# Optimization experiments

Measured on AMD Instinct MI355X. Metric: run time of the kernel, lower is better.

Reference implementation:

```python
import jax, jax.numpy as jnp
import numpy as np

MASK_WEIGHT = 1.0
HEAD_DIM = 64
SCALING = HEAD_DIM ** -0.5


def _rotate_half(x):
    x1, x2 = jnp.split(x, 2, axis=-1)
    return jnp.concatenate([-x2, x1], axis=-1)


def _rope_tables(seq_len, dim, dtype):
    inv_freq = 1.0 / (10000.0 ** (jnp.arange(0, dim, 2, dtype=jnp.float32) / dim))
    t = jnp.arange(seq_len, dtype=jnp.float32)
    freqs = jnp.outer(t, inv_freq)                      # (s, d/2)
    cos = jnp.tile(jnp.cos(freqs), (1, 2)).astype(dtype)  # (s, d)  '(2 d)' tiling
    sin = jnp.tile(jnp.sin(freqs), (1, 2)).astype(dtype)
    return cos, sin


def _apply_rope(x, cos, sin):
    # x: (b, h, s, d); cos/sin: (s, d) broadcast over b, h
    return x * cos + _rotate_half(x) * sin


def setup_inputs() -> dict:
    key = jax.random.key(0)
    ks = jax.random.split(key, 6)
    b, h, s, d = 2, 16, 2048, 64
    d_model = h * d
    return {
        "q": jax.random.normal(ks[0], (b, h, s, d), jnp.float32),
        "k": jax.random.normal(ks[1], (b, h, s, d), jnp.float32),
        "v": jax.random.normal(ks[2], (b, h, s, d), jnp.float32),
        "attention_mask": jax.random.normal(ks[3], (1, h, s, s), jnp.float32) * 0.05,
        "out_w": jax.random.normal(ks[4], (d_model, d_model), jnp.float32) * (d_model ** -0.5),
        "out_b": jax.random.normal(ks[5], (d_model,), jnp.float32) * 0.02,
    }


def reference(q, k, v, attention_mask, out_w, out_b):
    b, h, s, d = q.shape
    cos, sin = _rope_tables(s, d, q.dtype)
    qr = _apply_rope(q, cos, sin)
    kr = _apply_rope(k, cos, sin)
    # learned per-head affinity transform of the queries: q' = (mask_weight * W) @ q
    W = attention_mask[0] * MASK_WEIGHT                    # (h, s, s), shared over batch
    qt = jnp.einsum('hqk,bhkd->bhqd', W, qr)
    # flash-style online softmax over keys == plain stable softmax (same math)
    scores = jnp.einsum('bhqd,bhkd->bhqk', qt, kr) * SCALING
    attn = jax.nn.softmax(scores, axis=-1)
    ctx = jnp.einsum('bhqk,bhkd->bhqd', attn, v)
    ctx = ctx.transpose(0, 2, 1, 3).reshape(b, s, h * d)   # (b, s, d_model)
    return ctx @ out_w.T + out_b
```

## Files before the change

### kernel.cpp

```cpp
#include <hip/hip_runtime.h>
#include <hip/hip_bf16.h>
#include <math.h>

typedef __bf16 bf16_t;
typedef __bf16 bf16x4 __attribute__((ext_vector_type(4)));
typedef __bf16 bf16x8 __attribute__((ext_vector_type(8)));
typedef float f32x4 __attribute__((ext_vector_type(4)));

#define NB 2
#define NH 16
#define SEQ 2048
#define HD 64
#define DMODEL 1024
#define QK_SCALE 0.125f
#define LOG2E 1.44269504088896340f
#define INV_2PI 0.15915494309189535f

__device__ __forceinline__ bf16_t to_bf16(float x) { return (bf16_t)x; }
#define MFMA16 __builtin_amdgcn_mfma_f32_16x16x32_bf16

__global__ __launch_bounds__(256) void k1_rope_pack(
    const float* __restrict__ q, const float* __restrict__ k, const float* __restrict__ v,
    bf16_t* __restrict__ qrT, bf16_t* __restrict__ krN, bf16_t* __restrict__ vT)
{
  __shared__ bf16_t tile[64][65];
  const int tid = threadIdx.x;
  const int blk = blockIdx.x;
  const int st = blk & 31;
  const int bh = blk >> 5;
  const int s0 = st * 64;

  const size_t base_sd = ((size_t)bh * SEQ + s0) * HD;
  const float* qb = q + base_sd;
  const float* kb = k + base_sd;
  const float* vb = v + base_sd;
  bf16_t* qrTb = qrT + (size_t)bh * HD * SEQ;
  bf16_t* krNb = krN + base_sd;
  bf16_t* vTb  = vT  + (size_t)bh * HD * SEQ;

  #pragma unroll
  for (int pp = 0; pp < 8; ++pp) {
    int idx = pp * 256 + tid;
    int sr = idx >> 5;
    int j  = idx & 31;
    float freq = __builtin_amdgcn_exp2f(-(float)j * (13.287712379549449f / 32.0f));
    float ang = (float)(s0 + sr) * freq;
    float rev = ang * INV_2PI;
    rev = rev - floorf(rev);
    float c  = __builtin_amdgcn_cosf(rev);
    float sn = __builtin_amdgcn_sinf(rev);
    float q1 = qb[sr*HD + j], q2 = qb[sr*HD + j + 32];
    tile[sr][j]      = to_bf16((q1*c - q2*sn) * QK_SCALE);
    tile[sr][j + 32] = to_bf16((q2*c + q1*sn) * QK_SCALE);
    float ka = kb[sr*HD + j], kbv = kb[sr*HD + j + 32];
    krNb[sr*HD + j]      = to_bf16(ka*c - kbv*sn);
    krNb[sr*HD + j + 32] = to_bf16(kbv*c + ka*sn);
  }
  __syncthreads();
  #pragma unroll
  for (int c = 0; c < 2; ++c) {
    int id = c*256 + tid;
    int d = id >> 3;
    int sc = (id & 7) * 8;
    bf16x8 vec;
    #pragma unroll
    for (int i = 0; i < 8; ++i) vec[i] = tile[sc + i][d];
    *(bf16x8*)&qrTb[(size_t)d * SEQ + s0 + sc] = vec;
  }
  __syncthreads();
  #pragma unroll
  for (int c = 0; c < 4; ++c) {
    int id = c*256 + tid;
    int sr = id >> 4;
    int c4 = (id & 15) * 4;
    float4 v4 = *(const float4*)&vb[sr*HD + c4];
    tile[sr][c4+0] = to_bf16(v4.x);
    tile[sr][c4+1] = to_bf16(v4.y);
    tile[sr][c4+2] = to_bf16(v4.z);
    tile[sr][c4+3] = to_bf16(v4.w);
  }
  __syncthreads();
  #pragma unroll
  for (int c = 0; c < 2; ++c) {
    int id = c*256 + tid;
    int d = id >> 3;
    int sc = (id & 7) * 8;
    bf16x8 vec;
    #pragma unroll
    for (int i = 0; i < 8; ++i) vec[i] = tile[sc + i][d];
    *(bf16x8*)&vTb[(size_t)d * SEQ + s0 + sc] = vec;
  }
}

__global__ __launch_bounds__(256) void k2_qt_gemm(
    const float* __restrict__ Wm,
    const bf16_t* __restrict__ qrT,
    bf16_t* __restrict__ qtT)
{
  __shared__ __align__(16) bf16_t A_lds[2][64*40];
  __shared__ __align__(16) bf16_t B_lds[64*40];
  const int tid = threadIdx.x;
  const int blk = blockIdx.x;
  const int n0 = (blk & 31) * 64;
  const int h = blk >> 5;
  const int wave = tid >> 6, lane = tid & 63;
  const int l15 = lane & 15, quad = lane >> 4;
  const int r8 = tid >> 2, c8 = (tid & 3) * 8;

  const float* Wh = Wm + (size_t)h * SEQ * SEQ + (size_t)n0 * SEQ;
  f32x4 acc[2][4] = {};

  for (int kb = 0; kb < SEQ; kb += 32) {
    #pragma unroll
    for (int b2 = 0; b2 < 2; ++b2)
      *(bf16x8*)&A_lds[b2][r8*40 + c8] =
          *(const bf16x8*)&qrT[(((size_t)b2*NH + h)*HD + r8)*SEQ + kb + c8];
    float4 wa = *(const float4*)&Wh[(size_t)r8*SEQ + kb + c8];
    float4 wb = *(const float4*)&Wh[(size_t)r8*SEQ + kb + c8 + 4];
    bf16_t* dst = &B_lds[r8*40 + c8];
    dst[0]=to_bf16(wa.x); dst[1]=to_bf16(wa.y); dst[2]=to_bf16(wa.z); dst[3]=to_bf16(wa.w);
    dst[4]=to_bf16(wb.x); dst[5]=to_bf16(wb.y); dst[6]=to_bf16(wb.z); dst[7]=to_bf16(wb.w);
    __syncthreads();

    bf16x8 bfr[4];
    #pragma unroll
    for (int nt = 0; nt < 4; ++nt)
      bfr[nt] = *(const bf16x8*)&B_lds[(nt*16 + l15)*40 + quad*8];
    #pragma unroll
    for (int b2 = 0; b2 < 2; ++b2) {
      bf16x8 af = *(const bf16x8*)&A_lds[b2][(wave*16 + l15)*40 + quad*8];
      #pragma unroll
      for (int nt = 0; nt < 4; ++nt)
        acc[b2][nt] = MFMA16(af, bfr[nt], acc[b2][nt], 0, 0, 0);
    }
    __syncthreads();
  }
  #pragma unroll
  for (int b2 = 0; b2 < 2; ++b2)
    #pragma unroll
    for (int nt = 0; nt < 4; ++nt)
      #pragma unroll
      for (int r = 0; r < 4; ++r) {
        int d = wave*16 + quad*4 + r;
        qtT[(((size_t)b2*NH + h)*HD + d)*SEQ + n0 + nt*16 + l15] =
            to_bf16(acc[b2][nt][r] * LOG2E);
      }
}

__global__ __launch_bounds__(256, 2) void k3_flash(
    const bf16_t* __restrict__ qtT,
    const bf16_t* __restrict__ krN,
    const bf16_t* __restrict__ vT,
    bf16_t* __restrict__ ctx)
{
  __shared__ __align__(16) bf16_t K_lds[64*72];
  __shared__ __align__(16) bf16_t V_lds[64*72];
  __shared__ __align__(16) bf16_t P_lds[4][16*72];
  const int tid = threadIdx.x;
  const int blk = blockIdx.x;
  const int qt = blk & 15;
  const int bh = blk >> 4;
  const int h = bh & 15, b = bh >> 4;
  const int wave = tid >> 6, lane = tid & 63;
  const int l15 = lane & 15, quad = lane >> 4;
  const int qw = qt*128 + wave*32;

  const bf16_t* qtb = qtT + (size_t)bh * HD * SEQ;
  const bf16_t* krb = krN + (size_t)bh * SEQ * HD;
  const bf16_t* vtb = vT  + (size_t)bh * HD * SEQ;

  bf16x8 Qf[2][2];
  #pragma unroll
  for (int g = 0; g < 2; ++g)
    #pragma unroll
    for (int c = 0; c < 2; ++c)
      #pragma unroll
      for (int j = 0; j < 8; ++j)
        Qf[g][c][j] = qtb[(size_t)(c*32 + quad*8 + j)*SEQ + qw + g*16 + l15];

  bf16x8 ones;
  #pragma unroll
  for (int j = 0; j < 8; ++j) ones[j] = to_bf16(1.0f);

  f32x4 O[2][4] = {};
  f32x4 L[2] = {};

  for (int kt = 0; kt < 32; ++kt) {
    #pragma unroll
    for (int c = 0; c < 2; ++c) {
      int id = c*256 + tid;
      int row = id >> 3, ch = (id & 7) * 8;
      *(bf16x8*)&K_lds[row*72 + ch] = *(const bf16x8*)&krb[(size_t)(kt*64 + row)*HD + ch];
      *(bf16x8*)&V_lds[row*72 + ch] = *(const bf16x8*)&vtb[(size_t)row*SEQ + kt*64 + ch];
    }
    __syncthreads();

    bf16x8 ak[4][2], bv[4][2];
    #pragma unroll
    for (int nt = 0; nt < 4; ++nt) {
      ak[nt][0] = *(const bf16x8*)&K_lds[(nt*16 + l15)*72 + quad*8];
      ak[nt][1] = *(const bf16x8*)&K_lds[(nt*16 + l15)*72 + 32 + quad*8];
      bv[nt][0] = *(const bf16x8*)&V_lds[(nt*16 + l15)*72 + quad*8];
      bv[nt][1] = *(const bf16x8*)&V_lds[(nt*16 + l15)*72 + 32 + quad*8];
    }

    #pragma unroll
    for (int g = 0; g < 2; ++g) {
      f32x4 s[4] = {};
      #pragma unroll
      for (int nt = 0; nt < 4; ++nt) {
        s[nt] = MFMA16(ak[nt][0], Qf[g][0], s[nt], 0, 0, 0);
        s[nt] = MFMA16(ak[nt][1], Qf[g][1], s[nt], 0, 0, 0);
      }
      #pragma unroll
      for (int nt = 0; nt < 4; ++nt) {
        bf16x4 pk;
        #pragma unroll
        for (int r = 0; r < 4; ++r)
          pk[r] = to_bf16(__builtin_amdgcn_exp2f(s[nt][r]));
        *(bf16x4*)&P_lds[wave][l15*72 + nt*16 + quad*4] = pk;
      }
      bf16x8 ap0 = *(const bf16x8*)&P_lds[wave][l15*72 + quad*8];
      bf16x8 ap1 = *(const bf16x8*)&P_lds[wave][l15*72 + 32 + quad*8];
      #pragma unroll
      for (int nt = 0; nt < 4; ++nt) {
        O[g][nt] = MFMA16(ap0, bv[nt][0], O[g][nt], 0, 0, 0);
        O[g][nt] = MFMA16(ap1, bv[nt][1], O[g][nt], 0, 0, 0);
      }
      L[g] = MFMA16(ap0, ones, L[g], 0, 0, 0);
      L[g] = MFMA16(ap1, ones, L[g], 0, 0, 0);
    }
    __syncthreads();
  }

  #pragma unroll
  for (int g = 0; g < 2; ++g)
    #pragma unroll
    for (int nt = 0; nt < 4; ++nt)
      #pragma unroll
      for (int r = 0; r < 4; ++r) {
        int qrow = qw + g*16 + quad*4 + r;
        float o = O[g][nt][r] / L[g][r];
        ctx[((size_t)b*SEQ + qrow)*DMODEL + h*HD + nt*16 + l15] = to_bf16(o);
      }
}

__global__ __launch_bounds__(256) void k4_proj(
    const bf16_t* __restrict__ ctx,
    const float* __restrict__ w,
    const float* __restrict__ bias,
    float* __restrict__ out)
{
  __shared__ __align__(16) bf16_t A_lds[64*40];
  __shared__ __align__(16) bf16_t B_lds[64*40];
  const int tid = threadIdx.x;
  const int blk = blockIdx.x;
  const int n0 = (blk & 15) * 64;
  const int m0 = (blk >> 4) * 64;
  const int wave = tid >> 6, lane = tid & 63;
  const int l15 = lane & 15, quad = lane >> 4;
  const int r8 = tid >> 2, c8 = (tid & 3) * 8;

  f32x4 acc[4] = {};
  for (int kb = 0; kb < DMODEL; kb += 32) {
    *(bf16x8*)&A_lds[r8*40 + c8] = *(const bf16x8*)&ctx[(size_t)(m0 + r8)*DMODEL + kb + c8];
    float4 wa = *(const float4*)&w[(size_t)(n0 + r8)*DMODEL + kb + c8];
    float4 wb = *(const float4*)&w[(size_t)(n0 + r8)*DMODEL + kb + c8 + 4];
    bf16_t* dst = &B_lds[r8*40 + c8];
    dst[0]=to_bf16(wa.x); dst[1]=to_bf16(wa.y); dst[2]=to_bf16(wa.z); dst[3]=to_bf16(wa.w);
    dst[4]=to_bf16(wb.x); dst[5]=to_bf16(wb.y); dst[6]=to_bf16(wb.z); dst[7]=to_bf16(wb.w);
    __syncthreads();
    bf16x8 af = *(const bf16x8*)&A_lds[(wave*16 + l15)*40 + quad*8];
    #pragma unroll
    for (int nt = 0; nt < 4; ++nt) {
      bf16x8 bfr = *(const bf16x8*)&B_lds[(nt*16 + l15)*40 + quad*8];
      acc[nt] = MFMA16(af, bfr, acc[nt], 0, 0, 0);
    }
    __syncthreads();
  }
  #pragma unroll
  for (int nt = 0; nt < 4; ++nt) {
    float bb = bias[n0 + nt*16 + l15];
    #pragma unroll
    for (int r = 0; r < 4; ++r)
      out[(size_t)(m0 + wave*16 + quad*4 + r)*DMODEL + n0 + nt*16 + l15] = acc[nt][r] + bb;
  }
}

extern "C" void kernel_launch(void* const* d_in, const int* in_sizes, int n_in,
                              void* d_out, int out_size, void* d_ws, size_t ws_size,
                              hipStream_t stream)
{
  const float* q     = (const float*)d_in[0];
  const float* k     = (const float*)d_in[1];
  const float* v     = (const float*)d_in[2];
  const float* mask  = (const float*)d_in[3];
  const float* out_w = (const float*)d_in[4];
  const float* out_b = (const float*)d_in[5];
  float* out = (float*)d_out;

  const size_t elems = (size_t)NB * NH * SEQ * HD;
  bf16_t* qrT = (bf16_t*)d_ws;
  bf16_t* krN = qrT + elems;
  bf16_t* vT  = krN + elems;
  bf16_t* qtT = vT  + elems;
  bf16_t* ctx = qtT + elems;

  k1_rope_pack<<<dim3(NB*NH*(SEQ/64)), dim3(256), 0, stream>>>(q, k, v, qrT, krN, vT);
  k2_qt_gemm <<<dim3(NH*(SEQ/64)),     dim3(256), 0, stream>>>(mask, qrT, qtT);
  k3_flash   <<<dim3(NB*NH*(SEQ/128)), dim3(256), 0, stream>>>(qtT, krN, vT, ctx);
  k4_proj    <<<dim3((NB*SEQ/64)*(DMODEL/64)), dim3(256), 0, stream>>>(ctx, out_w, out_b, out);
}
```

Measured before the change: 535.8 us.

## Register-prefetch next tiles in GEMM and flash kernels, widen k-step and M-tile

k2, k3 and k4 now load the next K-tile from global memory into registers while MFMAs run on the current LDS tile. This replaces the load, sync, compute, sync pattern with a single barrier per iteration plus one before the LDS store. k2 and k4 also double the K-step to 64 with a padded stride of 72, and k4 doubles its M-tile to 128 rows so each W tile is reused twice and half as many blocks launch. This costs more registers and LDS per block, which may reduce occupancy.

```diff
diff --git a/kernel.cpp b/kernel.cpp
--- a/kernel.cpp
+++ b/kernel.cpp
@@ -97,43 +97,70 @@
     const bf16_t* __restrict__ qrT,
     bf16_t* __restrict__ qtT)
 {
-  __shared__ __align__(16) bf16_t A_lds[2][64*40];
-  __shared__ __align__(16) bf16_t B_lds[64*40];
+  __shared__ __align__(16) bf16_t A_lds[2][64*72];
+  __shared__ __align__(16) bf16_t B_lds[64*72];
   const int tid = threadIdx.x;
   const int blk = blockIdx.x;
   const int n0 = (blk & 31) * 64;
   const int h = blk >> 5;
   const int wave = tid >> 6, lane = tid & 63;
   const int l15 = lane & 15, quad = lane >> 4;
-  const int r8 = tid >> 2, c8 = (tid & 3) * 8;
+  const int rs = tid >> 2, cs = (tid & 3) * 16;
 
   const float* Wh = Wm + (size_t)h * SEQ * SEQ + (size_t)n0 * SEQ;
+  const bf16_t* A0 = qrT + ((size_t)h * HD + rs) * SEQ;
+  const bf16_t* A1 = qrT + (((size_t)NH + h) * HD + rs) * SEQ;
+
   f32x4 acc[2][4] = {};
-
-  for (int kb = 0; kb < SEQ; kb += 32) {
-    #pragma unroll
-    for (int b2 = 0; b2 < 2; ++b2)
-      *(bf16x8*)&A_lds[b2][r8*40 + c8] =
-          *(const bf16x8*)&qrT[(((size_t)b2*NH + h)*HD + r8)*SEQ + kb + c8];
-    float4 wa = *(const float4*)&Wh[(size_t)r8*SEQ + kb + c8];
-    float4 wb = *(const float4*)&Wh[(size_t)r8*SEQ + kb + c8 + 4];
-    bf16_t* dst = &B_lds[r8*40 + c8];
-    dst[0]=to_bf16(wa.x); dst[1]=to_bf16(wa.y); dst[2]=to_bf16(wa.z); dst[3]=to_bf16(wa.w);
-    dst[4]=to_bf16(wb.x); dst[5]=to_bf16(wb.y); dst[6]=to_bf16(wb.z); dst[7]=to_bf16(wb.w);
+  float4 wreg[4];
+  bf16x8 areg[2][2];
+
+  #pragma unroll
+  for (int i = 0; i < 4; ++i) wreg[i] = *(const float4*)&Wh[(size_t)rs*SEQ + cs + i*4];
+  #pragma unroll
+  for (int i = 0; i < 2; ++i) {
+    areg[0][i] = *(const bf16x8*)&A0[cs + i*8];
+    areg[1][i] = *(const bf16x8*)&A1[cs + i*8];
+  }
+
+  for (int it = 0; it < SEQ/64; ++it) {
+    if (it) __syncthreads();
+    #pragma unroll
+    for (int i = 0; i < 2; ++i) {
+      *(bf16x8*)&A_lds[0][rs*72 + cs + i*8] = areg[0][i];
+      *(bf16x8*)&A_lds[1][rs*72 + cs + i*8] = areg[1][i];
+      bf16x8 wb;
+      float4 wa = wreg[i*2], wc = wreg[i*2+1];
+      wb[0]=to_bf16(wa.x); wb[1]=to_bf16(wa.y); wb[2]=to_bf16(wa.z); wb[3]=to_bf16(wa.w);
+      wb[4]=to_bf16(wc.x); wb[5]=to_bf16(wc.y); wb[6]=to_bf16(wc.z); wb[7]=to_bf16(wc.w);
+      *(bf16x8*)&B_lds[rs*72 + cs + i*8] = wb;
+    }
     __syncthreads();
-
-    bf16x8 bfr[4];
-    #pragma unroll
-    for (int nt = 0; nt < 4; ++nt)
-      bfr[nt] = *(const bf16x8*)&B_lds[(nt*16 + l15)*40 + quad*8];
-    #pragma unroll
-    for (int b2 = 0; b2 < 2; ++b2) {
-      bf16x8 af = *(const bf16x8*)&A_lds[b2][(wave*16 + l15)*40 + quad*8];
+    if (it + 1 < SEQ/64) {
+      int kb = (it + 1) * 64;
+      #pragma unroll
+      for (int i = 0; i < 4; ++i) wreg[i] = *(const float4*)&Wh[(size_t)rs*SEQ + kb + cs + i*4];
+      #pragma unroll
+      for (int i = 0; i < 2; ++i) {
+        areg[0][i] = *(const bf16x8*)&A0[kb + cs + i*8];
+        areg[1][i] = *(const bf16x8*)&A1[kb + cs + i*8];
+      }
+    }
+    #pragma unroll
+    for (int kc = 0; kc < 2; ++kc) {
+      const int off = kc*32 + quad*8;
+      bf16x8 bfr[4];
       #pragma unroll
       for (int nt = 0; nt < 4; ++nt)
-        acc[b2][nt] = MFMA16(af, bfr[nt], acc[b2][nt], 0, 0, 0);
-    }
-    __syncthreads();
+        bfr[nt] = *(const bf16x8*)&B_lds[(nt*16 + l15)*72 + off];
+      #pragma unroll
+      for (int b2 = 0; b2 < 2; ++b2) {
+        bf16x8 af = *(const bf16x8*)&A_lds[b2][(wave*16 + l15)*72 + off];
+        #pragma unroll
+        for (int nt = 0; nt < 4; ++nt)
+          acc[b2][nt] = MFMA16(af, bfr[nt], acc[b2][nt], 0, 0, 0);
+      }
+    }
   }
   #pragma unroll
   for (int b2 = 0; b2 < 2; ++b2)
@@ -164,6 +191,7 @@
   const int wave = tid >> 6, lane = tid & 63;
   const int l15 = lane & 15, quad = lane >> 4;
   const int qw = qt*128 + wave*32;
+  const int srow = tid >> 3, sch = (tid & 7) * 8;
 
   const bf16_t* qtb = qtT + (size_t)bh * HD * SEQ;
   const bf16_t* krb = krN + (size_t)bh * SEQ * HD;
@@ -185,15 +213,31 @@
   f32x4 O[2][4] = {};
   f32x4 L[2] = {};
 
+  bf16x8 kreg[2], vreg[2];
+  #pragma unroll
+  for (int c = 0; c < 2; ++c) {
+    int row = c*32 + srow;
+    kreg[c] = *(const bf16x8*)&krb[(size_t)row*HD + sch];
+    vreg[c] = *(const bf16x8*)&vtb[(size_t)row*SEQ + sch];
+  }
+
   for (int kt = 0; kt < 32; ++kt) {
+    if (kt) __syncthreads();
     #pragma unroll
     for (int c = 0; c < 2; ++c) {
-      int id = c*256 + tid;
-      int row = id >> 3, ch = (id & 7) * 8;
-      *(bf16x8*)&K_lds[row*72 + ch] = *(const bf16x8*)&krb[(size_t)(kt*64 + row)*HD + ch];
-      *(bf16x8*)&V_lds[row*72 + ch] = *(const bf16x8*)&vtb[(size_t)row*SEQ + kt*64 + ch];
+      int row = c*32 + srow;
+      *(bf16x8*)&K_lds[row*72 + sch] = kreg[c];
+      *(bf16x8*)&V_lds[row*72 + sch] = vreg[c];
     }
     __syncthreads();
+    if (kt + 1 < 32) {
+      #pragma unroll
+      for (int c = 0; c < 2; ++c) {
+        int row = c*32 + srow;
+        kreg[c] = *(const bf16x8*)&krb[(size_t)((kt+1)*64 + row)*HD + sch];
+        vreg[c] = *(const bf16x8*)&vtb[(size_t)row*SEQ + (kt+1)*64 + sch];
+      }
+    }
 
     bf16x8 ak[4][2], bv[4][2];
     #pragma unroll
@@ -230,7 +274,6 @@
       L[g] = MFMA16(ap0, ones, L[g], 0, 0, 0);
       L[g] = MFMA16(ap1, ones, L[g], 0, 0, 0);
     }
-    __syncthreads();
   }
 
   #pragma unroll
@@ -251,39 +294,74 @@
     const float* __restrict__ bias,
     float* __restrict__ out)
 {
-  __shared__ __align__(16) bf16_t A_lds[64*40];
-  __shared__ __align__(16) bf16_t B_lds[64*40];
+  __shared__ __align__(16) bf16_t A_lds[128*72];
+  __shared__ __align__(16) bf16_t B_lds[64*72];
   const int tid = threadIdx.x;
   const int blk = blockIdx.x;
   const int n0 = (blk & 15) * 64;
-  const int m0 = (blk >> 4) * 64;
+  const int m0 = (blk >> 4) * 128;
   const int wave = tid >> 6, lane = tid & 63;
   const int l15 = lane & 15, quad = lane >> 4;
-  const int r8 = tid >> 2, c8 = (tid & 3) * 8;
-
-  f32x4 acc[4] = {};
-  for (int kb = 0; kb < DMODEL; kb += 32) {
-    *(bf16x8*)&A_lds[r8*40 + c8] = *(const bf16x8*)&ctx[(size_t)(m0 + r8)*DMODEL + kb + c8];
-    float4 wa = *(const float4*)&w[(size_t)(n0 + r8)*DMODEL + kb + c8];
-    float4 wb = *(const float4*)&w[(size_t)(n0 + r8)*DMODEL + kb + c8 + 4];
-    bf16_t* dst = &B_lds[r8*40 + c8];
-    dst[0]=to_bf16(wa.x); dst[1]=to_bf16(wa.y); dst[2]=to_bf16(wa.z); dst[3]=to_bf16(wa.w);
-    dst[4]=to_bf16(wb.x); dst[5]=to_bf16(wb.y); dst[6]=to_bf16(wb.z); dst[7]=to_bf16(wb.w);
+  const int ra = tid >> 1, ca = (tid & 1) * 32;
+  const int rs = tid >> 2, cs = (tid & 3) * 16;
+
+  f32x4 acc[2][4] = {};
+  bf16x8 areg[4];
+  float4 wreg[4];
+
+  #pragma unroll
+  for (int i = 0; i < 4; ++i) {
+    areg[i] = *(const bf16x8*)&ctx[(size_t)(m0 + ra)*DMODEL + ca + i*8];
+    wreg[i] = *(const float4*)&w[(size_t)(n0 + rs)*DMODEL + cs + i*4];
+  }
+
+  for (int it = 0; it < DMODEL/64; ++it) {
+    if (it) __syncthreads();
+    #pragma unroll
+    for (int i = 0; i < 4; ++i)
+      *(bf16x8*)&A_lds[ra*72 + ca + i*8] = areg[i];
+    #pragma unroll
+    for (int i = 0; i < 2; ++i) {
+      bf16x8 wb;
+      float4 wa = wreg[i*2], wc = wreg[i*2+1];
+      wb[0]=to_bf16(wa.x); wb[1]=to_bf16(wa.y); wb[2]=to_bf16(wa.z); wb[3]=to_bf16(wa.w);
+      wb[4]=to_bf16(wc.x); wb[5]=to_bf16(wc.y); wb[6]=to_bf16(wc.z); wb[7]=to_bf16(wc.w);
+      *(bf16x8*)&B_lds[rs*72 + cs + i*8] = wb;
+    }
     __syncthreads();
-    bf16x8 af = *(const bf16x8*)&A_lds[(wave*16 + l15)*40 + quad*8];
-    #pragma unroll
-    for (int nt = 0; nt < 4; ++nt) {
-      bf16x8 bfr = *(const bf16x8*)&B_lds[(nt*16 + l15)*40 + quad*8];
-      acc[nt] = MFMA16(af, bfr, acc[nt], 0, 0, 0);
-    }
-    __syncthreads();
+    if (it + 1 < DMODEL/64) {
+      int kb = (it + 1) * 64;
+      #pragma unroll
+      for (int i = 0; i < 4; ++i) {
+        areg[i] = *(const bf16x8*)&ctx[(size_t)(m0 + ra)*DMODEL + kb + ca + i*8];
+        wreg[i] = *(const float4*)&w[(size_t)(n0 + rs)*DMODEL + kb + cs + i*4];
+      }
+    }
+    #pragma unroll
+    for (int kc = 0; kc < 2; ++kc) {
+      const int off = kc*32 + quad*8;
+      bf16x8 bfr[4];
+      #pragma unroll
+      for (int nt = 0; nt < 4; ++nt)
+        bfr[nt] = *(const bf16x8*)&B_lds[(nt*16 + l15)*72 + off];
+      #pragma unroll
+      for (int g = 0; g < 2; ++g) {
+        bf16x8 af = *(const bf16x8*)&A_lds[(wave*32 + g*16 + l15)*72 + off];
+        #pragma unroll
+        for (int nt = 0; nt < 4; ++nt)
+          acc[g][nt] = MFMA16(af, bfr[nt], acc[g][nt], 0, 0, 0);
+      }
+    }
   }
   #pragma unroll
   for (int nt = 0; nt < 4; ++nt) {
     float bb = bias[n0 + nt*16 + l15];
     #pragma unroll
-    for (int r = 0; r < 4; ++r)
-      out[(size_t)(m0 + wave*16 + quad*4 + r)*DMODEL + n0 + nt*16 + l15] = acc[nt][r] + bb;
+    for (int g = 0; g < 2; ++g)
+      #pragma unroll
+      for (int r = 0; r < 4; ++r)
+        out[(size_t)(m0 + wave*32 + g*16 + quad*4 + r)*DMODEL + n0 + nt*16 + l15] =
+            acc[g][nt][r] + bb;
   }
 }
 
@@ -309,5 +387,5 @@
   k1_rope_pack<<<dim3(NB*NH*(SEQ/64)), dim3(256), 0, stream>>>(q, k, v, qrT, krN, vT);
   k2_qt_gemm <<<dim3(NH*(SEQ/64)),     dim3(256), 0, stream>>>(mask, qrT, qtT);
   k3_flash   <<<dim3(NB*NH*(SEQ/128)), dim3(256), 0, stream>>>(qtT, krN, vT, ctx);
-  k4_proj    <<<dim3((NB*SEQ/64)*(DMODEL/64)), dim3(256), 0, stream>>>(ctx, out_w, out_b, out);
-}
+  k4_proj    <<<dim3((NB*SEQ/128)*(DMODEL/64)), dim3(256), 0, stream>>>(ctx, out_w, out_b, out);
+}
```

Measured after the change: 487.3 us. 1.1x faster.
